# Optimization experiments

Hardware: AMD Instinct MI355X
Metric: run time of the kernel (lower is better)

Reference implementation:

```python
import jax, jax.numpy as jnp
import numpy as np

N, D, R, OUT, B = 4096, 128, 8, 128, 4096

def setup_inputs() -> dict:
    key = jax.random.key(0)
    ks = jax.random.split(key, 8)
    return {
        "embeddings": jax.random.normal(ks[0], (N, D), dtype=jnp.float32),
        "head_idx": jax.random.randint(ks[1], (B,), 0, N),
        "head_e": jax.random.normal(ks[2], (B, D), dtype=jnp.float32),
        "tail_idx": jax.random.randint(ks[3], (B,), 0, N),
        "tail_e": jax.random.normal(ks[4], (B, D), dtype=jnp.float32),
        "adj_mats": jax.random.uniform(ks[5], (R, N, N), dtype=jnp.float32),
        "relation_kernel": jax.random.normal(ks[6], (R, D, OUT), dtype=jnp.float32),
        "self_kernel": jax.random.normal(ks[7], (D, OUT), dtype=jnp.float32),
    }

def _branch(idx, e, adj_mats, embeddings, relation_kernel, self_kernel):
    # self transform: [B, OUT]
    out = e @ self_kernel
    # per-relation row gather: [R, B, N]
    adj = adj_mats[:, idx, :]
    # neighborhood aggregation: [R, B, D]
    upd = jnp.einsum('rbn,nd->rbd', adj, embeddings)
    # relation transform + accumulate over relations: [B, OUT]
    out = out + jnp.einsum('rbd,rdo->bo', upd, relation_kernel)
    return out

def reference(embeddings, head_idx, head_e, tail_idx, tail_e, adj_mats, relation_kernel, self_kernel):
    head_output = _branch(head_idx, head_e, adj_mats, embeddings, relation_kernel, self_kernel)
    tail_output = _branch(tail_idx, tail_e, adj_mats, embeddings, relation_kernel, self_kernel)
    return (head_output, tail_output)
```

## Files before the change

### kernel.cpp

```cpp
#include <hip/hip_runtime.h>

#define NN   4096
#define DD   128
#define RR   8
#define OUTD 128
#define BB   4096

typedef unsigned short ushort_t;
typedef __attribute__((ext_vector_type(8))) short short8;
typedef __attribute__((ext_vector_type(4))) float floatx4;

__device__ __forceinline__ ushort_t f2bf(float f) {
  union { float f; unsigned int u; } v; v.f = f;
  unsigned int u = v.u;
  return (ushort_t)((u + 0x7fffu + ((u >> 16) & 1u)) >> 16);
}

__device__ __forceinline__ unsigned int pk2(float x, float y) {
  union { float f; unsigned int u; } a, b;
  a.f = x; b.f = y;
  const unsigned int ua = a.u + 0x8000u;
  const unsigned int ub = b.u + 0x8000u;
  return __builtin_amdgcn_perm(ub, ua, 0x07060302u);
}

__device__ __forceinline__ short8 pack8(floatx4 a, floatx4 b) {
  union { unsigned int u[4]; short8 s; } r;
  r.u[0] = pk2(a[0], a[1]); r.u[1] = pk2(a[2], a[3]);
  r.u[2] = pk2(b[0], b[1]); r.u[3] = pk2(b[2], b[3]);
  return r.s;
}

__global__ __launch_bounds__(256) void compute_wt(const float* __restrict__ emb,
                                                  const float* __restrict__ rk,
                                                  ushort_t* __restrict__ Wt) {
  __shared__ float e_s[64][132];
  __shared__ float k_s[128][36];
  const int r  = blockIdx.y;
  const int m0 = blockIdx.x * 64;
  const int t  = threadIdx.x;
  {
    const int row = t >> 2, q = t & 3;
    const float* src = emb + (size_t)(m0 + row) * DD;
    #pragma unroll
    for (int j = 0; j < 8; ++j) {
      const int c = q + 4 * j;
      *(float4*)&e_s[row][c * 4] = *(const float4*)(src + c * 4);
    }
  }
  const int m_l = t >> 2, ob = (t & 3) * 8;
  const float* rkr = rk + (size_t)r * DD * OUTD;
  #pragma unroll 1
  for (int oc = 0; oc < 4; ++oc) {
    __syncthreads();
    {
      const int d = t >> 1, h = (t & 1) * 4;
      #pragma unroll
      for (int j = 0; j < 4; ++j) {
        const int c = h + j;
        *(float4*)&k_s[d][c * 4] = *(const float4*)(rkr + d * OUTD + oc * 32 + c * 4);
      }
    }
    __syncthreads();
    float acc[8] = {0, 0, 0, 0, 0, 0, 0, 0};
    #pragma unroll 4
    for (int d = 0; d < DD; ++d) {
      const float e  = e_s[m_l][d];
      const float4 w0 = *(const float4*)&k_s[d][ob];
      const float4 w1 = *(const float4*)&k_s[d][ob + 4];
      acc[0] += e * w0.x; acc[1] += e * w0.y; acc[2] += e * w0.z; acc[3] += e * w0.w;
      acc[4] += e * w1.x; acc[5] += e * w1.y; acc[6] += e * w1.z; acc[7] += e * w1.w;
    }
    ushort_t* dst = Wt + ((size_t)r * OUTD + oc * 32 + ob) * NN + m0 + m_l;
    #pragma unroll
    for (int j = 0; j < 8; ++j) dst[(size_t)j * NN] = f2bf(acc[j]);
  }
}

__global__ __launch_bounds__(256, 2) void rgcn_main(const float* __restrict__ adj,
                                                    const ushort_t* __restrict__ Wt,
                                                    float* __restrict__ Zr) {
  __shared__ short8 B8[2][2048];
  const int r  = blockIdx.y;
  const int n0 = blockIdx.x * 64;
  const int t = threadIdx.x;
  const int lane = t & 63, wave = t >> 6;
  const int l15 = lane & 15, l4 = lane >> 4;
  const float* __restrict__ arow =
      adj + (size_t)r * NN * NN + (size_t)(n0 + wave * 16 + l15) * NN;
  const ushort_t* __restrict__ wtr = Wt + (size_t)r * OUTD * NN;

  floatx4 acc[8] = {};
  floatx4 av[8];
  short8  af[4];

  auto stageB = [&](int buf, int k0) {
    #pragma unroll
    for (int it = 0; it < 8; ++it) {
      const int s = wave * 512 + it * 64 + lane;
      const int o = s >> 4, kc = s & 15;
      const int gkc = kc ^ (o & 15);
      const ushort_t* gp = wtr + (size_t)o * NN + k0 + gkc * 8;
      __builtin_amdgcn_global_load_lds(
          (const __attribute__((address_space(1))) void*)gp,
          (__attribute__((address_space(3))) void*)&B8[buf][wave * 512 + it * 64],
          16, 0, 0);
    }
  };
  auto loadA = [&](int k0) {
    #pragma unroll
    for (int kk = 0; kk < 4; ++kk) {
      const floatx4* p = (const floatx4*)(arow + k0 + kk * 32 + l4 * 8);
      av[2 * kk]     = __builtin_nontemporal_load(p);
      av[2 * kk + 1] = __builtin_nontemporal_load(p + 1);
    }
  };

  stageB(0, 0);
  loadA(0);
  __syncthreads();

  int cur = 0;
  #pragma unroll 1
  for (int kt = 0; kt < 32; ++kt) {
    if (kt + 1 < 32) stageB(cur ^ 1, (kt + 1) * 128);
    #pragma unroll
    for (int kk = 0; kk < 4; ++kk) af[kk] = pack8(av[2 * kk], av[2 * kk + 1]);
    if (kt + 1 < 32) loadA((kt + 1) * 128);
    #pragma unroll
    for (int kk = 0; kk < 4; ++kk) {
      short8 bf[8];
      #pragma unroll
      for (int tj = 0; tj < 8; ++tj) {
        const int orow = tj * 16 + l15;
        bf[tj] = B8[cur][orow * 16 + ((kk * 4 + l4) ^ (orow & 15))];
      }
      #pragma unroll
      for (int tj = 0; tj < 8; ++tj)
        acc[tj] = __builtin_amdgcn_mfma_f32_16x16x32_bf16(af[kk], bf[tj],
                                                          acc[tj], 0, 0, 0);
    }
    __syncthreads();
    cur ^= 1;
  }

  float* zout = Zr + ((size_t)r * NN + n0 + wave * 16) * OUTD;
  #pragma unroll
  for (int tj = 0; tj < 8; ++tj)
    #pragma unroll
    for (int j = 0; j < 4; ++j)
      zout[(size_t)(l4 * 4 + j) * OUTD + tj * 16 + l15] = acc[tj][j];
}

__global__ __launch_bounds__(256) void epilogue_k(const float* __restrict__ he,
                                                  const float* __restrict__ te,
                                                  const int* __restrict__ hidx,
                                                  const int* __restrict__ tidx,
                                                  const float* __restrict__ sk,
                                                  const float* __restrict__ Zr,
                                                  float* __restrict__ out) {
  __shared__ float e_s[64][132];
  __shared__ float k_s[128][36];
  const int bx = blockIdx.x;
  const int branch = bx >> 6;
  const int row0 = (bx & 63) * 64;
  const float* e  = branch ? te : he;
  const int* idx  = branch ? tidx : hidx;
  float* ob = out + (size_t)branch * BB * OUTD;
  const int t = threadIdx.x;
  {
    const int row = t >> 2, q = t & 3;
    const float* src = e + (size_t)(row0 + row) * DD;
    #pragma unroll
    for (int j = 0; j < 8; ++j) {
      const int c = q + 4 * j;
      *(float4*)&e_s[row][c * 4] = *(const float4*)(src + c * 4);
    }
  }
  const int m_l = t >> 2, obk = (t & 3) * 8;
  const int zi = idx[row0 + m_l];
  #pragma unroll 1
  for (int oc = 0; oc < 4; ++oc) {
    __syncthreads();
    {
      const int d = t >> 1, h = (t & 1) * 4;
      #pragma unroll
      for (int j = 0; j < 4; ++j) {
        const int c = h + j;
        *(float4*)&k_s[d][c * 4] = *(const float4*)(sk + d * OUTD + oc * 32 + c * 4);
      }
    }
    __syncthreads();
    float acc[8] = {0, 0, 0, 0, 0, 0, 0, 0};
    #pragma unroll 4
    for (int d = 0; d < DD; ++d) {
      const float ev = e_s[m_l][d];
      const float4 w0 = *(const float4*)&k_s[d][obk];
      const float4 w1 = *(const float4*)&k_s[d][obk + 4];
      acc[0] += ev * w0.x; acc[1] += ev * w0.y; acc[2] += ev * w0.z; acc[3] += ev * w0.w;
      acc[4] += ev * w1.x; acc[5] += ev * w1.y; acc[6] += ev * w1.z; acc[7] += ev * w1.w;
    }
    floatx4 z0 = {0.f, 0.f, 0.f, 0.f}, z1 = {0.f, 0.f, 0.f, 0.f};
    #pragma unroll
    for (int rr = 0; rr < RR; ++rr) {
      const float* zrow = Zr + ((size_t)rr * NN + zi) * OUTD + oc * 32;
      z0 += *(const floatx4*)(zrow + obk);
      z1 += *(const floatx4*)(zrow + obk + 4);
    }
    floatx4 o0, o1;
    o0[0] = acc[0] + z0[0]; o0[1] = acc[1] + z0[1];
    o0[2] = acc[2] + z0[2]; o0[3] = acc[3] + z0[3];
    o1[0] = acc[4] + z1[0]; o1[1] = acc[5] + z1[1];
    o1[2] = acc[6] + z1[2]; o1[3] = acc[7] + z1[3];
    *(floatx4*)&ob[(size_t)(row0 + m_l) * OUTD + oc * 32 + obk]     = o0;
    *(floatx4*)&ob[(size_t)(row0 + m_l) * OUTD + oc * 32 + obk + 4] = o1;
  }
}

extern "C" void kernel_launch(void* const* d_in, const int* in_sizes, int n_in,
                              void* d_out, int out_size, void* d_ws, size_t ws_size,
                              hipStream_t stream) {
  const float* emb  = (const float*)d_in[0];
  const int*   hidx = (const int*)  d_in[1];
  const float* he   = (const float*)d_in[2];
  const int*   tidx = (const int*)  d_in[3];
  const float* te   = (const float*)d_in[4];
  const float* adj  = (const float*)d_in[5];
  const float* rk   = (const float*)d_in[6];
  const float* sk   = (const float*)d_in[7];
  float* out = (float*)d_out;

  ushort_t* Wt = (ushort_t*)d_ws;
  float*    Zr = (float*)((char*)d_ws + (size_t)RR * OUTD * NN * sizeof(ushort_t));

  compute_wt<<<dim3(64, 8), 256, 0, stream>>>(emb, rk, Wt);
  rgcn_main<<<dim3(64, 8), 256, 0, stream>>>(adj, Wt, Zr);
  epilogue_k<<<dim3(128), 256, 0, stream>>>(he, te, hidx, tidx, sk, Zr, out);
}
```

Before: 750.1 us.

## Aggregate only adjacency rows referenced by head/tail indices via compacted row list

Adds a single-block kernel that marks which node rows appear in head_idx or tail_idx. It builds a compacted row list plus an inverse map. The main GEMM now multiplies only those gathered adjacency rows, and the epilogue reads results through the inverse map. This skips reading and multiplying adjacency rows that are never used. The A operand is also staged into LDS with async global_load_lds and swizzling, using a smaller 64-wide k-tile. It adds a serial prologue kernel and an indirect row gather, and the grid is sized for the worst case, with early exit.

```diff
diff --git a/kernel.cpp b/kernel.cpp
--- a/kernel.cpp
+++ b/kernel.cpp
@@ -29,6 +29,37 @@
   r.u[0] = pk2(a[0], a[1]); r.u[1] = pk2(a[2], a[3]);
   r.u[2] = pk2(b[0], b[1]); r.u[3] = pk2(b[2], b[3]);
   return r.s;
+}
+
+__global__ __launch_bounds__(1024) void build_rows(const int* __restrict__ hidx,
+                                                   const int* __restrict__ tidx,
+                                                   int* __restrict__ cnt,
+                                                   int* __restrict__ rows,
+                                                   int* __restrict__ inv,
+                                                   int* __restrict__ flags) {
+  __shared__ int lcnt;
+  const int t = threadIdx.x;
+  if (t == 0) lcnt = 0;
+  #pragma unroll
+  for (int j = 0; j < 4; ++j) flags[t + j * 1024] = 0;
+  __syncthreads();
+  #pragma unroll
+  for (int j = 0; j < 4; ++j) {
+    flags[hidx[t + j * 1024]] = 1;
+    flags[tidx[t + j * 1024]] = 1;
+  }
+  __syncthreads();
+  #pragma unroll
+  for (int j = 0; j < 4; ++j) {
+    const int rrow = t + j * 1024;
+    if (flags[rrow]) {
+      const int p = atomicAdd(&lcnt, 1);
+      rows[p]   = rrow;
+      inv[rrow] = p;
+    }
+  }
+  __syncthreads();
+  if (t == 0) *cnt = lcnt;
 }
 
 __global__ __launch_bounds__(256) void compute_wt(const float* __restrict__ emb,
@@ -79,72 +110,83 @@
 
 __global__ __launch_bounds__(256, 2) void rgcn_main(const float* __restrict__ adj,
                                                     const ushort_t* __restrict__ Wt,
-                                                    float* __restrict__ Zr) {
-  __shared__ short8 B8[2][2048];
-  const int r  = blockIdx.y;
-  const int n0 = blockIdx.x * 64;
+                                                    float* __restrict__ Zc,
+                                                    const int* __restrict__ cntp,
+                                                    const int* __restrict__ rowsp) {
+  __shared__ floatx4 A4[2][1024];
+  __shared__ short8  B8[2][1024];
+  const int cnt = cntp[0];
+  const int bid = blockIdx.x;
+  const int r   = bid & 7;
+  const int ci0 = (bid >> 3) * 64;
+  if (ci0 >= cnt) return;
   const int t = threadIdx.x;
   const int lane = t & 63, wave = t >> 6;
   const int l15 = lane & 15, l4 = lane >> 4;
-  const float* __restrict__ arow =
-      adj + (size_t)r * NN * NN + (size_t)(n0 + wave * 16 + l15) * NN;
-  const ushort_t* __restrict__ wtr = Wt + (size_t)r * OUTD * NN;
+  const float*    __restrict__ adjr = adj + (size_t)r * NN * NN;
+  const ushort_t* __restrict__ wtr  = Wt + (size_t)r * OUTD * NN;
+
+  const float*    abase[4];
+  const ushort_t* bbase[4];
+  #pragma unroll
+  for (int it = 0; it < 4; ++it) {
+    const int s  = it * 256 + wave * 64 + lane;
+    {
+      const int rw = s >> 4, c = s & 15;
+      const int ci = ci0 + rw;
+      const int grow = (ci < cnt) ? rowsp[ci] : rowsp[ci0];
+      abase[it] = adjr + (size_t)grow * NN + (c ^ (rw & 15)) * 4;
+    }
+    {
+      const int rw = s >> 3, c = s & 7;
+      bbase[it] = wtr + (size_t)rw * NN + (c ^ (rw & 7)) * 8;
+    }
+  }
+
+  auto stageA = [&](int buf, int k0) {
+    #pragma unroll
+    for (int it = 0; it < 4; ++it)
+      __builtin_amdgcn_global_load_lds(
+          (const __attribute__((address_space(1))) void*)(abase[it] + k0),
+          (__attribute__((address_space(3))) void*)&A4[buf][it * 256 + wave * 64],
+          16, 0, 0);
+  };
+  auto stageB = [&](int buf, int k0) {
+    #pragma unroll
+    for (int it = 0; it < 4; ++it)
+      __builtin_amdgcn_global_load_lds(
+          (const __attribute__((address_space(1))) void*)(bbase[it] + k0),
+          (__attribute__((address_space(3))) void*)&B8[buf][it * 256 + wave * 64],
+          16, 0, 0);
+  };
 
   floatx4 acc[8] = {};
-  floatx4 av[8];
-  short8  af[4];
-
-  auto stageB = [&](int buf, int k0) {
-    #pragma unroll
-    for (int it = 0; it < 8; ++it) {
-      const int s = wave * 512 + it * 64 + lane;
-      const int o = s >> 4, kc = s & 15;
-      const int gkc = kc ^ (o & 15);
-      const ushort_t* gp = wtr + (size_t)o * NN + k0 + gkc * 8;
-      __builtin_amdgcn_global_load_lds(
-          (const __attribute__((address_space(1))) void*)gp,
-          (__attribute__((address_space(3))) void*)&B8[buf][wave * 512 + it * 64],
-          16, 0, 0);
-    }
-  };
-  auto loadA = [&](int k0) {
-    #pragma unroll
-    for (int kk = 0; kk < 4; ++kk) {
-      const floatx4* p = (const floatx4*)(arow + k0 + kk * 32 + l4 * 8);
-      av[2 * kk]     = __builtin_nontemporal_load(p);
-      av[2 * kk + 1] = __builtin_nontemporal_load(p + 1);
-    }
-  };
-
-  stageB(0, 0);
-  loadA(0);
-  __syncthreads();
-
+  stageA(0, 0); stageB(0, 0);
+  __syncthreads();
+
+  const int lrow = wave * 16 + l15;
   int cur = 0;
   #pragma unroll 1
-  for (int kt = 0; kt < 32; ++kt) {
-    if (kt + 1 < 32) stageB(cur ^ 1, (kt + 1) * 128);
-    #pragma unroll
-    for (int kk = 0; kk < 4; ++kk) af[kk] = pack8(av[2 * kk], av[2 * kk + 1]);
-    if (kt + 1 < 32) loadA((kt + 1) * 128);
-    #pragma unroll
-    for (int kk = 0; kk < 4; ++kk) {
-      short8 bf[8];
+  for (int kt = 0; kt < 64; ++kt) {
+    if (kt + 1 < 64) { stageA(cur ^ 1, (kt + 1) * 64); stageB(cur ^ 1, (kt + 1) * 64); }
+    #pragma unroll
+    for (int kk = 0; kk < 2; ++kk) {
+      const int cc = kk * 8 + l4 * 2;
+      const floatx4 alo = A4[cur][lrow * 16 + ((cc)     ^ (lrow & 15))];
+      const floatx4 ahi = A4[cur][lrow * 16 + ((cc + 1) ^ (lrow & 15))];
+      const short8 af = pack8(alo, ahi);
       #pragma unroll
       for (int tj = 0; tj < 8; ++tj) {
         const int orow = tj * 16 + l15;
-        bf[tj] = B8[cur][orow * 16 + ((kk * 4 + l4) ^ (orow & 15))];
+        const short8 bf = B8[cur][orow * 8 + ((kk * 4 + l4) ^ (orow & 7))];
+        acc[tj] = __builtin_amdgcn_mfma_f32_16x16x32_bf16(af, bf, acc[tj], 0, 0, 0);
       }
-      #pragma unroll
-      for (int tj = 0; tj < 8; ++tj)
-        acc[tj] = __builtin_amdgcn_mfma_f32_16x16x32_bf16(af[kk], bf[tj],
-                                                          acc[tj], 0, 0, 0);
     }
     __syncthreads();
     cur ^= 1;
   }
 
-  float* zout = Zr + ((size_t)r * NN + n0 + wave * 16) * OUTD;
+  float* zout = Zc + ((size_t)r * NN + ci0 + wave * 16) * OUTD;
   #pragma unroll
   for (int tj = 0; tj < 8; ++tj)
     #pragma unroll
@@ -157,7 +199,8 @@
                                                   const int* __restrict__ hidx,
                                                   const int* __restrict__ tidx,
                                                   const float* __restrict__ sk,
-                                                  const float* __restrict__ Zr,
+                                                  const float* __restrict__ Zc,
+                                                  const int* __restrict__ invp,
                                                   float* __restrict__ out) {
   __shared__ float e_s[64][132];
   __shared__ float k_s[128][36];
@@ -179,6 +222,7 @@
   }
   const int m_l = t >> 2, obk = (t & 3) * 8;
   const int zi = idx[row0 + m_l];
+  const int ci = invp[zi];
   #pragma unroll 1
   for (int oc = 0; oc < 4; ++oc) {
     __syncthreads();
@@ -203,7 +247,7 @@
     floatx4 z0 = {0.f, 0.f, 0.f, 0.f}, z1 = {0.f, 0.f, 0.f, 0.f};
     #pragma unroll
     for (int rr = 0; rr < RR; ++rr) {
-      const float* zrow = Zr + ((size_t)rr * NN + zi) * OUTD + oc * 32;
+      const float* zrow = Zc + ((size_t)rr * NN + ci) * OUTD + oc * 32;
       z0 += *(const floatx4*)(zrow + obk);
       z1 += *(const floatx4*)(zrow + obk + 4);
     }
@@ -231,9 +275,15 @@
   float* out = (float*)d_out;
 
   ushort_t* Wt = (ushort_t*)d_ws;
-  float*    Zr = (float*)((char*)d_ws + (size_t)RR * OUTD * NN * sizeof(ushort_t));
-
+  float*    Zc = (float*)((char*)d_ws + (size_t)RR * OUTD * NN * sizeof(ushort_t));
+  int* meta  = (int*)((char*)d_ws + (size_t)24 * 1024 * 1024);
+  int* cnt   = meta;
+  int* rows  = meta + 16;
+  int* inv   = rows + NN;
+  int* flags = inv + NN;
+
+  build_rows<<<dim3(1), 1024, 0, stream>>>(hidx, tidx, cnt, rows, inv, flags);
   compute_wt<<<dim3(64, 8), 256, 0, stream>>>(emb, rk, Wt);
-  rgcn_main<<<dim3(64, 8), 256, 0, stream>>>(adj, Wt, Zr);
-  epilogue_k<<<dim3(128), 256, 0, stream>>>(he, te, hidx, tidx, sk, Zr, out);
-}
+  rgcn_main<<<dim3(512), 256, 0, stream>>>(adj, Wt, Zc, cnt, rows);
+  epilogue_k<<<dim3(128), 256, 0, stream>>>(he, te, hidx, tidx, sk, Zc, inv, out);
+}
```

Result: slower. 766.8 us (+2.2%).

## Compute adjacency aggregation only for rows referenced by head/tail indices

Applied to the files above, without the earlier changes.

A new single-block kernel marks which node rows are referenced by head_idx or tail_idx and compacts them into a row list with an inverse map. The main MFMA kernel then streams only those compacted adjacency rows, and blocks past the unique count exit early. The epilogue reads results through the inverse map. This avoids reading and multiplying adjacency rows that no output uses, at the cost of an extra small serial launch and gathered row addressing.

```diff
diff --git a/kernel.cpp b/kernel.cpp
--- a/kernel.cpp
+++ b/kernel.cpp
@@ -29,6 +29,37 @@
   r.u[0] = pk2(a[0], a[1]); r.u[1] = pk2(a[2], a[3]);
   r.u[2] = pk2(b[0], b[1]); r.u[3] = pk2(b[2], b[3]);
   return r.s;
+}
+
+__global__ __launch_bounds__(1024) void build_rows(const int* __restrict__ hidx,
+                                                   const int* __restrict__ tidx,
+                                                   int* __restrict__ cnt,
+                                                   int* __restrict__ rows,
+                                                   int* __restrict__ inv,
+                                                   int* __restrict__ flags) {
+  __shared__ int lcnt;
+  const int t = threadIdx.x;
+  if (t == 0) lcnt = 0;
+  #pragma unroll
+  for (int j = 0; j < 4; ++j) flags[t + j * 1024] = 0;
+  __syncthreads();
+  #pragma unroll
+  for (int j = 0; j < 4; ++j) {
+    flags[hidx[t + j * 1024]] = 1;
+    flags[tidx[t + j * 1024]] = 1;
+  }
+  __syncthreads();
+  #pragma unroll
+  for (int j = 0; j < 4; ++j) {
+    const int rrow = t + j * 1024;
+    if (flags[rrow]) {
+      const int p = atomicAdd(&lcnt, 1);
+      rows[p]   = rrow;
+      inv[rrow] = p;
+    }
+  }
+  __syncthreads();
+  if (t == 0) *cnt = lcnt;
 }
 
 __global__ __launch_bounds__(256) void compute_wt(const float* __restrict__ emb,
@@ -79,15 +110,20 @@
 
 __global__ __launch_bounds__(256, 2) void rgcn_main(const float* __restrict__ adj,
                                                     const ushort_t* __restrict__ Wt,
-                                                    float* __restrict__ Zr) {
+                                                    float* __restrict__ Zc,
+                                                    const int* __restrict__ cntp,
+                                                    const int* __restrict__ rowsp) {
   __shared__ short8 B8[2][2048];
-  const int r  = blockIdx.y;
-  const int n0 = blockIdx.x * 64;
+  const int cnt = cntp[0];
+  const int r   = blockIdx.y;
+  const int ci0 = blockIdx.x * 64;
+  if (ci0 >= cnt) return;
   const int t = threadIdx.x;
   const int lane = t & 63, wave = t >> 6;
   const int l15 = lane & 15, l4 = lane >> 4;
-  const float* __restrict__ arow =
-      adj + (size_t)r * NN * NN + (size_t)(n0 + wave * 16 + l15) * NN;
+  const int ci   = ci0 + wave * 16 + l15;
+  const int grow = rowsp[ci < cnt ? ci : cnt - 1];
+  const float* __restrict__ arow = adj + (size_t)r * NN * NN + (size_t)grow * NN;
   const ushort_t* __restrict__ wtr = Wt + (size_t)r * OUTD * NN;
 
   floatx4 acc[8] = {};
@@ -144,7 +180,7 @@
     cur ^= 1;
   }
 
-  float* zout = Zr + ((size_t)r * NN + n0 + wave * 16) * OUTD;
+  float* zout = Zc + ((size_t)r * NN + ci0 + wave * 16) * OUTD;
   #pragma unroll
   for (int tj = 0; tj < 8; ++tj)
     #pragma unroll
@@ -157,7 +193,8 @@
                                                   const int* __restrict__ hidx,
                                                   const int* __restrict__ tidx,
                                                   const float* __restrict__ sk,
-                                                  const float* __restrict__ Zr,
+                                                  const float* __restrict__ Zc,
+                                                  const int* __restrict__ invp,
                                                   float* __restrict__ out) {
   __shared__ float e_s[64][132];
   __shared__ float k_s[128][36];
@@ -179,6 +216,7 @@
   }
   const int m_l = t >> 2, obk = (t & 3) * 8;
   const int zi = idx[row0 + m_l];
+  const int ci = invp[zi];
   #pragma unroll 1
   for (int oc = 0; oc < 4; ++oc) {
     __syncthreads();
@@ -203,7 +241,7 @@
     floatx4 z0 = {0.f, 0.f, 0.f, 0.f}, z1 = {0.f, 0.f, 0.f, 0.f};
     #pragma unroll
     for (int rr = 0; rr < RR; ++rr) {
-      const float* zrow = Zr + ((size_t)rr * NN + zi) * OUTD + oc * 32;
+      const float* zrow = Zc + ((size_t)rr * NN + ci) * OUTD + oc * 32;
       z0 += *(const floatx4*)(zrow + obk);
       z1 += *(const floatx4*)(zrow + obk + 4);
     }
@@ -231,9 +269,15 @@
   float* out = (float*)d_out;
 
   ushort_t* Wt = (ushort_t*)d_ws;
-  float*    Zr = (float*)((char*)d_ws + (size_t)RR * OUTD * NN * sizeof(ushort_t));
-
+  float*    Zc = (float*)((char*)d_ws + (size_t)RR * OUTD * NN * sizeof(ushort_t));
+  int* meta  = (int*)((char*)d_ws + (size_t)24 * 1024 * 1024);
+  int* cnt   = meta;
+  int* rows  = meta + 16;
+  int* inv   = rows + NN;
+  int* flags = inv + NN;
+
+  build_rows<<<dim3(1), 1024, 0, stream>>>(hidx, tidx, cnt, rows, inv, flags);
   compute_wt<<<dim3(64, 8), 256, 0, stream>>>(emb, rk, Wt);
-  rgcn_main<<<dim3(64, 8), 256, 0, stream>>>(adj, Wt, Zr);
-  epilogue_k<<<dim3(128), 256, 0, stream>>>(he, te, hidx, tidx, sk, Zr, out);
-}
+  rgcn_main<<<dim3(64, 8), 256, 0, stream>>>(adj, Wt, Zc, cnt, rows);
+  epilogue_k<<<dim3(128), 256, 0, stream>>>(he, te, hidx, tidx, sk, Zc, inv, out);
+}
```

Measured after the change: 766.3 us. 2.2% more time.
